# Performance work log

Measured on AMD Instinct MI355X. Metric: run time of the kernel, lower is better.

## Reference

```python
import jax, jax.numpy as jnp
import numpy as np

# Human3.6M 17-joint skeleton (parent of each joint; -1 = root)
_PARENTS = np.array([-1, 0, 1, 2, 0, 4, 5, 0, 7, 8, 9, 8, 11, 12, 8, 14, 15])
J = 17          # joints
C_OUT = 128     # out_features (per-channel adjacency count)
F_IN = 128      # in_features
B, T = 64, 243  # batch, frames
NEG = -9.0e15   # matches torch constant -9000000000000000.0


def _skeleton_indices():
    A = np.eye(J, dtype=np.float32)  # self-loops (SemGCN adjacency includes I)
    for i, p in enumerate(_PARENTS):
        if p >= 0:
            A[i, p] = 1.0
            A[p, i] = 1.0
    ii, jj = np.nonzero(A)  # row-major order, identical to torch adj>0 mask order
    return ii.astype(np.int32), jj.astype(np.int32)


def setup_inputs() -> dict:
    key = jax.random.key(0)
    kx, kw, ke = jax.random.split(key, 3)
    ii, jj = _skeleton_indices()  # nnz = 49
    x = jax.random.normal(kx, (B, T, J, F_IN), dtype=jnp.float32)
    # xavier_uniform with gain=1.414 over (2, in, out)
    bound = 1.414 * np.sqrt(6.0 / (F_IN + C_OUT))
    W = jax.random.uniform(kw, (2, F_IN, C_OUT), dtype=jnp.float32,
                           minval=-bound, maxval=bound)
    e = jax.random.uniform(ke, (C_OUT, ii.shape[0]), dtype=jnp.float32)
    return {"x": x, "W": W, "e": e,
            "idx_i": jnp.asarray(ii), "idx_j": jnp.asarray(jj)}


def reference(x, W, e, idx_i, idx_j):
    # x: [B,T,J,F_in], W: [2,F_in,C], e: [C,nnz]
    C = e.shape[0]
    nj = x.shape[2]
    h0 = jnp.einsum('btji,io->btjo', x, W[0])  # [B,T,J,C]
    h1 = jnp.einsum('btji,io->btjo', x, W[1])  # [B,T,J,C]
    # dense per-channel adjacency: masked scatter of e, then row softmax
    adj = jnp.full((C, nj, nj), NEG, dtype=x.dtype)
    adj = adj.at[:, idx_i, idx_j].set(e)
    adj = jax.nn.softmax(adj, axis=2)  # [C,J,J]
    # diagonal part: (adj*E) @ h0  ==  elementwise scale by diag entries
    d = jnp.diagonal(adj, axis1=1, axis2=2)        # [C,J]
    eye = jnp.eye(nj, dtype=x.dtype)
    off = adj * (1.0 - eye)                         # [C,J,J]
    out = h0 * d.T[None, None] + jnp.einsum('cjk,btkc->btjc', off, h1)
    return out  # [B,T,J,C]
```

## Files before the change

### kernel.cpp

```cpp
#include <hip/hip_runtime.h>

#define NJ   17
#define FD   128
#define NC   128
#define NNZ  49
#define FPT  16
#define XROW (NJ*FD)
#define WS_WT 65536

typedef __attribute__((ext_vector_type(8))) short bf16x8;
typedef __attribute__((ext_vector_type(4))) float f32x4;

__device__ __forceinline__ ushort f2bf(float f) {
  unsigned u = __float_as_uint(f);
  u = (u + 0x7fffu + ((u >> 16) & 1u)) >> 16;
  return (ushort)u;
}
__device__ __forceinline__ float bf2f(ushort s) {
  return __uint_as_float(((unsigned)s) << 16);
}
__device__ __forceinline__ unsigned cvtpk(float a, float b) {
  unsigned r;
  asm("v_cvt_pk_bf16_f32 %0, %1, %2" : "=v"(r) : "v"(a), "v"(b));
  return r;
}
__device__ __forceinline__ bf16x8 pack8(float4 a, float4 b) {
  union { unsigned u[4]; bf16x8 v; } r;
  r.u[0] = cvtpk(a.x, a.y); r.u[1] = cvtpk(a.z, a.w);
  r.u[2] = cvtpk(b.x, b.y); r.u[3] = cvtpk(b.z, b.w);
  return r.v;
}
__device__ __forceinline__ void axpy(f32x4& o, float s, f32x4 h) {
  o[0] += s * h[0]; o[1] += s * h[1]; o[2] += s * h[2]; o[3] += s * h[3];
}

struct CI { int col, dk, n, jl[3], kk[3]; };
constexpr CI TAB0[9] = {
  {0,  0, 3, {1,4,7}, {4,12,20}},
  {1,  5, 2, {0,2,0}, {1,7,0}},
  {2,  8, 2, {1,3,0}, {6,10,0}},
  {3, 11, 1, {2,0,0}, {9,0,0}},
  {4, 13, 2, {0,5,0}, {2,15,0}},
  {5, 16, 2, {4,6,0}, {14,18,0}},
  {6, 19, 1, {5,0,0}, {17,0,0}},
  {7, 21, 1, {0,0,0}, {3,0,0}},
  {8, -1, 1, {7,0,0}, {22,0,0}},
};
constexpr CI TAB1[10] = {
  {7, -1, 1, {0,0,0}, {23,0,0}},
  {8, 24, 3, {1,3,6}, {28,33,41}},
  {9, 29, 2, {0,2,0}, {25,31,0}},
  {10,32, 1, {1,0,0}, {30,0,0}},
  {11,34, 2, {0,4,0}, {26,36,0}},
  {12,37, 2, {3,5,0}, {35,39,0}},
  {13,40, 1, {4,0,0}, {38,0,0}},
  {14,42, 2, {0,7,0}, {27,44,0}},
  {15,45, 2, {6,8,0}, {43,47,0}},
  {16,48, 1, {7,0,0}, {46,0,0}},
};
constexpr int RP[NJ + 1] = {0,4,7,10,12,15,18,20,23,28,31,33,36,39,41,44,47,49};

__global__ void prep_pack_kernel(const float* __restrict__ W,
                                 const float* __restrict__ e,
                                 bf16x8* __restrict__ Wpack,
                                 ushort* __restrict__ wt) {
  const int tid = threadIdx.x;
  if (blockIdx.x < 16) {
    const int idx = blockIdx.x * 256 + tid, n = idx >> 4, kb = idx & 15;
    const float* Wp = W + (size_t)(n >> 7) * (FD * NC) + (n & 127);
    bf16x8 v;
#pragma unroll
    for (int q = 0; q < 8; ++q) v[q] = (short)f2bf(Wp[(size_t)(kb * 8 + q) * NC]);
    Wpack[idx] = v;
  } else if (tid < NC) {
    const int c = tid;
    for (int j = 0; j < NJ; ++j) {
      const int k0 = RP[j], k1 = RP[j + 1];
      float m = -1e30f;
      for (int k = k0; k < k1; ++k) m = fmaxf(m, e[c * NNZ + k]);
      float s = 0.f;
      for (int k = k0; k < k1; ++k) s += expf(e[c * NNZ + k] - m);
      const float inv = 1.f / s;
      for (int k = k0; k < k1; ++k) wt[c * 64 + k] = f2bf(expf(e[c * NNZ + k] - m) * inv);
    }
    for (int k = NNZ; k < 64; ++k) wt[c * 64 + k] = 0;
  }
}

template <int HALF>
__device__ __forceinline__ void half_work(const float* __restrict__ xt,
                                          float* __restrict__ ob,
                                          const bf16x8* __restrict__ Wpack,
                                          const ushort* __restrict__ wt,
                                          short* xs, int tid) {
  constexpr int COL0 = HALF ? 7 : 0;
  constexpr int NCOL = HALF ? 10 : 9;
  constexpr int JN   = HALF ? 9 : 8;
  constexpr int JB   = HALF ? 8 : 0;
  constexpr int NCI  = HALF ? 10 : 9;
  constexpr int NGRP = FPT * NCOL * 16;
  const CI* TT = HALF ? TAB1 : TAB0;

  const int w = tid >> 6, lane = tid & 63, l15 = lane & 15, l4 = lane >> 4;
  const int cb = w * 16;
  const int c  = cb + l15;

  float4 v[10];
#pragma unroll
  for (int i = 0; i < 5; ++i) {
    const int g = tid + i * 512;
    if (NGRP % 512 == 0 || g < NGRP) {
      const int fr = g / (NCOL * 16), rem = g - fr * (NCOL * 16);
      const float* sp = xt + (size_t)fr * XROW + COL0 * FD + rem * 8;
      v[2 * i]     = *(const float4*)(sp);
      v[2 * i + 1] = *(const float4*)(sp + 4);
    }
  }

  bf16x8 bfr[2][4];
#pragma unroll
  for (int sel = 0; sel < 2; ++sel)
#pragma unroll
    for (int ks = 0; ks < 4; ++ks)
      bfr[sel][ks] = Wpack[(sel * 128 + c) * 16 + ks * 4 + l4];
  bf16x8 wtp[7];
#pragma unroll
  for (int r = 0; r < 7; ++r)
    wtp[r] = *(const bf16x8*)(wt + c * 64 + r * 8);

#pragma unroll
  for (int i = 0; i < 5; ++i) {
    const int g = tid + i * 512;
    if (NGRP % 512 == 0 || g < NGRP) {
      const int fr = g / (NCOL * 16);
      const int byte = (g * 16) ^ ((fr & 7) << 4);
      *(bf16x8*)((char*)xs + byte) = pack8(v[2 * i], v[2 * i + 1]);
    }
  }
  __syncthreads();

  f32x4 oa[JN];
#pragma unroll
  for (int j = 0; j < JN; ++j) oa[j] = (f32x4){0.f, 0.f, 0.f, 0.f};

#pragma unroll
  for (int ci = 0; ci < NCI; ++ci) {
    const int lc = TT[ci].col - COL0, dk = TT[ci].dk, nn = TT[ci].n;
    bf16x8 af[4];
#pragma unroll
    for (int ks = 0; ks < 4; ++ks) {
      const int byte = l15 * (NCOL * 256) + lc * 256 +
                       (((ks * 4 + l4) * 16) ^ ((l15 & 7) << 4));
      af[ks] = *(const bf16x8*)((const char*)xs + byte);
    }
    f32x4 h1 = (f32x4){0.f, 0.f, 0.f, 0.f};
#pragma unroll
    for (int ks = 0; ks < 4; ++ks)
      h1 = __builtin_amdgcn_mfma_f32_16x16x32_bf16(af[ks], bfr[1][ks], h1, 0, 0, 0);
    if (dk >= 0) {
      f32x4 h0 = (f32x4){0.f, 0.f, 0.f, 0.f};
#pragma unroll
      for (int ks = 0; ks < 4; ++ks)
        h0 = __builtin_amdgcn_mfma_f32_16x16x32_bf16(af[ks], bfr[0][ks], h0, 0, 0, 0);
      axpy(oa[TT[ci].col - JB], bf2f((ushort)wtp[dk >> 3][dk & 7]), h0);
    }
#pragma unroll
    for (int o = 0; o < 3; ++o)
      if (o < nn)
        axpy(oa[TT[ci].jl[o]], bf2f((ushort)wtp[TT[ci].kk[o] >> 3][TT[ci].kk[o] & 7]), h1);
  }

#pragma unroll
  for (int j = 0; j < JN; ++j)
#pragma unroll
    for (int q = 0; q < 4; ++q)
      ob[(size_t)(l4 * 4 + q) * XROW + (JB + j) * FD + c] = oa[j][q];
}

__global__ __launch_bounds__(512, 4) void fused_kernel(
    const float*  __restrict__ x,
    const bf16x8* __restrict__ Wpack,
    const ushort* __restrict__ wt,
    float*        __restrict__ out) {
  __shared__ __align__(16) short xs[FPT * 10 * FD];
  const int tile = blockIdx.x >> 1;
  const float* xt = x + (size_t)tile * (FPT * XROW);
  float* ob = out + (size_t)tile * (FPT * XROW);
  if (blockIdx.x & 1) half_work<1>(xt, ob, Wpack, wt, xs, threadIdx.x);
  else                half_work<0>(xt, ob, Wpack, wt, xs, threadIdx.x);
}

extern "C" void kernel_launch(void* const* d_in, const int* in_sizes, int n_in,
                              void* d_out, int out_size, void* d_ws, size_t ws_size,
                              hipStream_t stream) {
  const float* x = (const float*)d_in[0];
  const float* W = (const float*)d_in[1];
  const float* e = (const float*)d_in[2];
  float* out = (float*)d_out;

  bf16x8* Wpack = (bf16x8*)d_ws;
  ushort* wt    = (ushort*)((char*)d_ws + WS_WT);

  prep_pack_kernel<<<17, 256, 0, stream>>>(W, e, Wpack, wt);

  const int frames = in_sizes[0] / XROW;
  const int ntiles = frames / FPT;
  fused_kernel<<<ntiles * 2, 512, 0, stream>>>(x, Wpack, wt, out);
}
```

Measured before the change: 99.81 us.

## Process two tiles per block with register prefetch of the next tile

Measured after the change: 163.0 us. 1.63x slower.

```diff
diff --git a/kernel.cpp b/kernel.cpp
--- a/kernel.cpp
+++ b/kernel.cpp
@@ -6,6 +6,7 @@
 #define NNZ  49
 #define FPT  16
 #define XROW (NJ*FD)
+#define TPB  2
 #define WS_WT 65536
 
 typedef __attribute__((ext_vector_type(8))) short bf16x8;
@@ -33,6 +34,12 @@
 __device__ __forceinline__ void axpy(f32x4& o, float s, f32x4 h) {
   o[0] += s * h[0]; o[1] += s * h[1]; o[2] += s * h[2]; o[3] += s * h[3];
 }
+
+#define BAR() do {                                          \
+    asm volatile("s_waitcnt lgkmcnt(0)" ::: "memory");      \
+    __builtin_amdgcn_s_barrier();                           \
+    __builtin_amdgcn_sched_barrier(0);                      \
+  } while (0)
 
 struct CI { int col, dk, n, jl[3], kk[3]; };
 constexpr CI TAB0[9] = {
@@ -88,34 +95,20 @@
 }
 
 template <int HALF>
-__device__ __forceinline__ void half_work(const float* __restrict__ xt,
-                                          float* __restrict__ ob,
-                                          const bf16x8* __restrict__ Wpack,
-                                          const ushort* __restrict__ wt,
-                                          short* xs, int tid) {
+__device__ __forceinline__ void body(const float* __restrict__ x,
+                                     const bf16x8* __restrict__ Wpack,
+                                     const ushort* __restrict__ wt,
+                                     float* __restrict__ out,
+                                     short* xs, int slot, int tid) {
   constexpr int COL0 = HALF ? 7 : 0;
   constexpr int NCOL = HALF ? 10 : 9;
   constexpr int JN   = HALF ? 9 : 8;
   constexpr int JB   = HALF ? 8 : 0;
-  constexpr int NCI  = HALF ? 10 : 9;
   constexpr int NGRP = FPT * NCOL * 16;
   const CI* TT = HALF ? TAB1 : TAB0;
 
   const int w = tid >> 6, lane = tid & 63, l15 = lane & 15, l4 = lane >> 4;
-  const int cb = w * 16;
-  const int c  = cb + l15;
-
-  float4 v[10];
-#pragma unroll
-  for (int i = 0; i < 5; ++i) {
-    const int g = tid + i * 512;
-    if (NGRP % 512 == 0 || g < NGRP) {
-      const int fr = g / (NCOL * 16), rem = g - fr * (NCOL * 16);
-      const float* sp = xt + (size_t)fr * XROW + COL0 * FD + rem * 8;
-      v[2 * i]     = *(const float4*)(sp);
-      v[2 * i + 1] = *(const float4*)(sp + 4);
-    }
-  }
+  const int c = w * 16 + l15;
 
   bf16x8 bfr[2][4];
 #pragma unroll
@@ -128,53 +121,85 @@
   for (int r = 0; r < 7; ++r)
     wtp[r] = *(const bf16x8*)(wt + c * 64 + r * 8);
 
-#pragma unroll
-  for (int i = 0; i < 5; ++i) {
-    const int g = tid + i * 512;
-    if (NGRP % 512 == 0 || g < NGRP) {
-      const int fr = g / (NCOL * 16);
-      const int byte = (g * 16) ^ ((fr & 7) << 4);
-      *(bf16x8*)((char*)xs + byte) = pack8(v[2 * i], v[2 * i + 1]);
+  float4 v[10];
+
+#define LOADX(T) do {                                                     \
+    const float* xp_ = x + (size_t)(T) * (FPT * XROW) + COL0 * FD;        \
+    _Pragma("unroll")                                                     \
+    for (int i_ = 0; i_ < 5; ++i_) {                                      \
+      int g_ = tid + i_ * 512;                                            \
+      if (g_ > NGRP - 1) g_ = NGRP - 1;                                   \
+      const int fr_ = g_ / (NCOL * 16), rem_ = g_ - fr_ * (NCOL * 16);    \
+      const float* sp_ = xp_ + (size_t)fr_ * XROW + rem_ * 8;             \
+      v[2 * i_]     = *(const float4*)(sp_);                              \
+      v[2 * i_ + 1] = *(const float4*)(sp_ + 4);                          \
+    }                                                                     \
+  } while (0)
+
+#define STAGE() do {                                                      \
+    _Pragma("unroll")                                                     \
+    for (int i_ = 0; i_ < 5; ++i_) {                                      \
+      const int g_ = tid + i_ * 512;                                      \
+      if (NGRP % 512 == 0 || g_ < NGRP) {                                 \
+        const int fr_ = g_ / (NCOL * 16);                                 \
+        const int byte_ = (g_ * 16) ^ ((fr_ & 7) << 4);                   \
+        *(bf16x8*)((char*)xs + byte_) = pack8(v[2 * i_], v[2 * i_ + 1]);  \
+      }                                                                   \
+    }                                                                     \
+  } while (0)
+
+  const int t0 = slot * TPB;
+  LOADX(t0);
+
+#pragma unroll
+  for (int i = 0; i < TPB; ++i) {
+    const int t = t0 + i;
+
+    BAR();
+    STAGE();
+    BAR();
+    if (i + 1 < TPB) LOADX(t + 1);
+
+    f32x4 oa[JN];
+#pragma unroll
+    for (int j = 0; j < JN; ++j) oa[j] = (f32x4){0.f, 0.f, 0.f, 0.f};
+
+#pragma unroll
+    for (int ci = 0; ci < NCOL; ++ci) {
+      const int lc = TT[ci].col - COL0, dk = TT[ci].dk, nn = TT[ci].n;
+      bf16x8 af[4];
+#pragma unroll
+      for (int ks = 0; ks < 4; ++ks) {
+        const int byte = l15 * (NCOL * 256) + lc * 256 +
+                         (((ks * 4 + l4) * 16) ^ ((l15 & 7) << 4));
+        af[ks] = *(const bf16x8*)((const char*)xs + byte);
+      }
+      f32x4 h1 = (f32x4){0.f, 0.f, 0.f, 0.f};
+#pragma unroll
+      for (int ks = 0; ks < 4; ++ks)
+        h1 = __builtin_amdgcn_mfma_f32_16x16x32_bf16(af[ks], bfr[1][ks], h1, 0, 0, 0);
+      if (dk >= 0) {
+        f32x4 h0 = (f32x4){0.f, 0.f, 0.f, 0.f};
+#pragma unroll
+        for (int ks = 0; ks < 4; ++ks)
+          h0 = __builtin_amdgcn_mfma_f32_16x16x32_bf16(af[ks], bfr[0][ks], h0, 0, 0, 0);
+        axpy(oa[TT[ci].col - JB], bf2f((ushort)wtp[dk >> 3][dk & 7]), h0);
+      }
+#pragma unroll
+      for (int o = 0; o < 3; ++o)
+        if (o < nn)
+          axpy(oa[TT[ci].jl[o]], bf2f((ushort)wtp[TT[ci].kk[o] >> 3][TT[ci].kk[o] & 7]), h1);
     }
+
+    float* ob = out + (size_t)t * (FPT * XROW);
+#pragma unroll
+    for (int j = 0; j < JN; ++j)
+#pragma unroll
+      for (int q = 0; q < 4; ++q)
+        ob[(size_t)(l4 * 4 + q) * XROW + (JB + j) * FD + c] = oa[j][q];
   }
-  __syncthreads();
-
-  f32x4 oa[JN];
-#pragma unroll
-  for (int j = 0; j < JN; ++j) oa[j] = (f32x4){0.f, 0.f, 0.f, 0.f};
-
-#pragma unroll
-  for (int ci = 0; ci < NCI; ++ci) {
-    const int lc = TT[ci].col - COL0, dk = TT[ci].dk, nn = TT[ci].n;
-    bf16x8 af[4];
-#pragma unroll
-    for (int ks = 0; ks < 4; ++ks) {
-      const int byte = l15 * (NCOL * 256) + lc * 256 +
-                       (((ks * 4 + l4) * 16) ^ ((l15 & 7) << 4));
-      af[ks] = *(const bf16x8*)((const char*)xs + byte);
-    }
-    f32x4 h1 = (f32x4){0.f, 0.f, 0.f, 0.f};
-#pragma unroll
-    for (int ks = 0; ks < 4; ++ks)
-      h1 = __builtin_amdgcn_mfma_f32_16x16x32_bf16(af[ks], bfr[1][ks], h1, 0, 0, 0);
-    if (dk >= 0) {
-      f32x4 h0 = (f32x4){0.f, 0.f, 0.f, 0.f};
-#pragma unroll
-      for (int ks = 0; ks < 4; ++ks)
-        h0 = __builtin_amdgcn_mfma_f32_16x16x32_bf16(af[ks], bfr[0][ks], h0, 0, 0, 0);
-      axpy(oa[TT[ci].col - JB], bf2f((ushort)wtp[dk >> 3][dk & 7]), h0);
-    }
-#pragma unroll
-    for (int o = 0; o < 3; ++o)
-      if (o < nn)
-        axpy(oa[TT[ci].jl[o]], bf2f((ushort)wtp[TT[ci].kk[o] >> 3][TT[ci].kk[o] & 7]), h1);
-  }
-
-#pragma unroll
-  for (int j = 0; j < JN; ++j)
-#pragma unroll
-    for (int q = 0; q < 4; ++q)
-      ob[(size_t)(l4 * 4 + q) * XROW + (JB + j) * FD + c] = oa[j][q];
+#undef LOADX
+#undef STAGE
 }
 
 __global__ __launch_bounds__(512, 4) void fused_kernel(
@@ -183,11 +208,9 @@
     const ushort* __restrict__ wt,
     float*        __restrict__ out) {
   __shared__ __align__(16) short xs[FPT * 10 * FD];
-  const int tile = blockIdx.x >> 1;
-  const float* xt = x + (size_t)tile * (FPT * XROW);
-  float* ob = out + (size_t)tile * (FPT * XROW);
-  if (blockIdx.x & 1) half_work<1>(xt, ob, Wpack, wt, xs, threadIdx.x);
-  else                half_work<0>(xt, ob, Wpack, wt, xs, threadIdx.x);
+  const int slot = blockIdx.x >> 1;
+  if (blockIdx.x & 1) body<1>(x, Wpack, wt, out, xs, slot, threadIdx.x);
+  else                body<0>(x, Wpack, wt, out, xs, slot, threadIdx.x);
 }
 
 extern "C" void kernel_launch(void* const* d_in, const int* in_sizes, int n_in,
@@ -205,5 +228,6 @@
 
   const int frames = in_sizes[0] / XROW;
   const int ntiles = frames / FPT;
-  fused_kernel<<<ntiles * 2, 512, 0, stream>>>(x, Wpack, wt, out);
-}
+  const int blocks = (ntiles / TPB) * 2;
+  fused_kernel<<<blocks, 512, 0, stream>>>(x, Wpack, wt, out);
+}
```

## Double-buffer x tiles via global_load_lds across K-quarters and two tiles per block

Applied to the files above, without the earlier changes.

After: 223.1 us. 123% more time.

```diff
diff --git a/kernel.cpp b/kernel.cpp
--- a/kernel.cpp
+++ b/kernel.cpp
@@ -6,6 +6,8 @@
 #define NNZ  49
 #define FPT  16
 #define XROW (NJ*FD)
+#define TPB  2
+#define BUFB 20736
 #define WS_WT 65536
 
 typedef __attribute__((ext_vector_type(8))) short bf16x8;
@@ -24,15 +26,21 @@
   asm("v_cvt_pk_bf16_f32 %0, %1, %2" : "=v"(r) : "v"(a), "v"(b));
   return r;
 }
-__device__ __forceinline__ bf16x8 pack8(float4 a, float4 b) {
+__device__ __forceinline__ bf16x8 pack8(f32x4 a, f32x4 b) {
   union { unsigned u[4]; bf16x8 v; } r;
-  r.u[0] = cvtpk(a.x, a.y); r.u[1] = cvtpk(a.z, a.w);
-  r.u[2] = cvtpk(b.x, b.y); r.u[3] = cvtpk(b.z, b.w);
+  r.u[0] = cvtpk(a[0], a[1]); r.u[1] = cvtpk(a[2], a[3]);
+  r.u[2] = cvtpk(b[0], b[1]); r.u[3] = cvtpk(b[2], b[3]);
   return r.v;
 }
 __device__ __forceinline__ void axpy(f32x4& o, float s, f32x4 h) {
   o[0] += s * h[0]; o[1] += s * h[1]; o[2] += s * h[2]; o[3] += s * h[3];
 }
+
+#define WVM(N) do { asm volatile("s_waitcnt vmcnt(" #N ")" ::: "memory"); \
+                    __builtin_amdgcn_sched_barrier(0); } while (0)
+#define BARR() do { asm volatile("s_waitcnt lgkmcnt(0)" ::: "memory"); \
+                    __builtin_amdgcn_s_barrier(); \
+                    __builtin_amdgcn_sched_barrier(0); } while (0)
 
 struct CI { int col, dk, n, jl[3], kk[3]; };
 constexpr CI TAB0[9] = {
@@ -87,81 +95,27 @@
   }
 }
 
-template <int HALF>
-__device__ __forceinline__ void half_work(const float* __restrict__ xt,
-                                          float* __restrict__ ob,
-                                          const bf16x8* __restrict__ Wpack,
-                                          const ushort* __restrict__ wt,
-                                          short* xs, int tid) {
+template <int HALF, int P, int JN>
+__device__ __forceinline__ void cphase(const char* bb, int foff, int l4,
+                                       const bf16x8 (&bfr)[2][4],
+                                       const bf16x8 (&wtp)[7],
+                                       f32x4 (&oa)[JN]) {
+  constexpr int KQ   = P & 3;
   constexpr int COL0 = HALF ? 7 : 0;
   constexpr int NCOL = HALF ? 10 : 9;
-  constexpr int JN   = HALF ? 9 : 8;
   constexpr int JB   = HALF ? 8 : 0;
-  constexpr int NCI  = HALF ? 10 : 9;
-  constexpr int NGRP = FPT * NCOL * 16;
   const CI* TT = HALF ? TAB1 : TAB0;
-
-  const int w = tid >> 6, lane = tid & 63, l15 = lane & 15, l4 = lane >> 4;
-  const int cb = w * 16;
-  const int c  = cb + l15;
-
-  float4 v[10];
-#pragma unroll
-  for (int i = 0; i < 5; ++i) {
-    const int g = tid + i * 512;
-    if (NGRP % 512 == 0 || g < NGRP) {
-      const int fr = g / (NCOL * 16), rem = g - fr * (NCOL * 16);
-      const float* sp = xt + (size_t)fr * XROW + COL0 * FD + rem * 8;
-      v[2 * i]     = *(const float4*)(sp);
-      v[2 * i + 1] = *(const float4*)(sp + 4);
-    }
-  }
-
-  bf16x8 bfr[2][4];
-#pragma unroll
-  for (int sel = 0; sel < 2; ++sel)
-#pragma unroll
-    for (int ks = 0; ks < 4; ++ks)
-      bfr[sel][ks] = Wpack[(sel * 128 + c) * 16 + ks * 4 + l4];
-  bf16x8 wtp[7];
-#pragma unroll
-  for (int r = 0; r < 7; ++r)
-    wtp[r] = *(const bf16x8*)(wt + c * 64 + r * 8);
-
-#pragma unroll
-  for (int i = 0; i < 5; ++i) {
-    const int g = tid + i * 512;
-    if (NGRP % 512 == 0 || g < NGRP) {
-      const int fr = g / (NCOL * 16);
-      const int byte = (g * 16) ^ ((fr & 7) << 4);
-      *(bf16x8*)((char*)xs + byte) = pack8(v[2 * i], v[2 * i + 1]);
-    }
-  }
-  __syncthreads();
-
-  f32x4 oa[JN];
-#pragma unroll
-  for (int j = 0; j < JN; ++j) oa[j] = (f32x4){0.f, 0.f, 0.f, 0.f};
-
-#pragma unroll
-  for (int ci = 0; ci < NCI; ++ci) {
+  const char* fb = bb + foff;
+#pragma unroll
+  for (int ci = 0; ci < NCOL; ++ci) {
     const int lc = TT[ci].col - COL0, dk = TT[ci].dk, nn = TT[ci].n;
-    bf16x8 af[4];
-#pragma unroll
-    for (int ks = 0; ks < 4; ++ks) {
-      const int byte = l15 * (NCOL * 256) + lc * 256 +
-                       (((ks * 4 + l4) * 16) ^ ((l15 & 7) << 4));
-      af[ks] = *(const bf16x8*)((const char*)xs + byte);
-    }
-    f32x4 h1 = (f32x4){0.f, 0.f, 0.f, 0.f};
-#pragma unroll
-    for (int ks = 0; ks < 4; ++ks)
-      h1 = __builtin_amdgcn_mfma_f32_16x16x32_bf16(af[ks], bfr[1][ks], h1, 0, 0, 0);
+    const f32x4 lo = *(const f32x4*)(fb + lc * 128 + l4 * 32);
+    const f32x4 hi = *(const f32x4*)(fb + lc * 128 + l4 * 32 + 16);
+    const bf16x8 af = pack8(lo, hi);
+    const f32x4 z = (f32x4){0.f, 0.f, 0.f, 0.f};
+    const f32x4 h1 = __builtin_amdgcn_mfma_f32_16x16x32_bf16(af, bfr[1][KQ], z, 0, 0, 0);
     if (dk >= 0) {
-      f32x4 h0 = (f32x4){0.f, 0.f, 0.f, 0.f};
-#pragma unroll
-      for (int ks = 0; ks < 4; ++ks)
-        h0 = __builtin_amdgcn_mfma_f32_16x16x32_bf16(af[ks], bfr[0][ks], h0, 0, 0, 0);
+      const f32x4 h0 = __builtin_amdgcn_mfma_f32_16x16x32_bf16(af, bfr[0][KQ], z, 0, 0, 0);
       axpy(oa[TT[ci].col - JB], bf2f((ushort)wtp[dk >> 3][dk & 7]), h0);
     }
 #pragma unroll
@@ -169,12 +123,101 @@
       if (o < nn)
         axpy(oa[TT[ci].jl[o]], bf2f((ushort)wtp[TT[ci].kk[o] >> 3][TT[ci].kk[o] & 7]), h1);
   }
-
-#pragma unroll
-  for (int j = 0; j < JN; ++j)
-#pragma unroll
-    for (int q = 0; q < 4; ++q)
-      ob[(size_t)(l4 * 4 + q) * XROW + (JB + j) * FD + c] = oa[j][q];
+}
+
+template <int HALF>
+__device__ __forceinline__ void run(const float* __restrict__ x,
+                                    const bf16x8* __restrict__ Wpack,
+                                    const ushort* __restrict__ wt,
+                                    float* __restrict__ out,
+                                    char* xs, int slot, int tid) {
+  constexpr int COL0 = HALF ? 7 : 0;
+  constexpr int JN   = HALF ? 9 : 8;
+  constexpr int JB   = HALF ? 8 : 0;
+  const int w = tid >> 6, lane = tid & 63, l15 = lane & 15, l4 = lane >> 4;
+  const int c = w * 16 + l15;
+
+  bf16x8 bfr[2][4];
+#pragma unroll
+  for (int sel = 0; sel < 2; ++sel)
+#pragma unroll
+    for (int ks = 0; ks < 4; ++ks)
+      bfr[sel][ks] = Wpack[(sel * 128 + c) * 16 + ks * 4 + l4];
+  bf16x8 wtp[7];
+#pragma unroll
+  for (int r = 0; r < 7; ++r)
+    wtp[r] = *(const bf16x8*)(wt + c * 64 + r * 8);
+
+  f32x4 oa[JN];
+#pragma unroll
+  for (int j = 0; j < JN; ++j) oa[j] = (f32x4){0.f, 0.f, 0.f, 0.f};
+
+  const int foff = HALF ? l15 * 1296 : (l15 >> 1) * 2320 + (l15 & 1) * 1152;
+
+  auto issue = [&](int p) {
+    const int t = p >> 2, kq = p & 3;
+    char* dst = xs + (p & 1) * BUFB;
+    const float* gf0 = x + ((size_t)(slot * TPB + t) * FPT + 2 * w) * XROW +
+                       COL0 * FD + kq * 32;
+    const float* gf1 = gf0 + XROW;
+    if (HALF) {
+      char* d0 = dst + (2 * w) * 1296;
+      __builtin_amdgcn_global_load_lds(gf0 + (lane >> 3) * FD + (lane & 7) * 4,
+                                       (void*)d0, 16, 0, 0);
+      __builtin_amdgcn_global_load_lds(gf0 + (8 + (lane >> 5)) * FD + (lane & 31),
+                                       (void*)(d0 + 1024), 4, 0, 0);
+      __builtin_amdgcn_global_load_lds(gf1 + (lane >> 3) * FD + (lane & 7) * 4,
+                                       (void*)(d0 + 1296), 16, 0, 0);
+      __builtin_amdgcn_global_load_lds(gf1 + (8 + (lane >> 5)) * FD + (lane & 31),
+                                       (void*)(d0 + 1296 + 1024), 4, 0, 0);
+    } else {
+      char* pb = dst + w * 2320;
+      const float* s2 = (lane < 8)
+          ? gf0 + 8 * FD + lane * 4
+          : gf1 + ((lane * 16 - 128) >> 7) * FD + (((lane * 16 - 128) & 127) >> 2);
+      __builtin_amdgcn_global_load_lds(gf0 + (lane >> 3) * FD + (lane & 7) * 4,
+                                       (void*)pb, 16, 0, 0);
+      __builtin_amdgcn_global_load_lds(s2, (void*)(pb + 1024), 16, 0, 0);
+      __builtin_amdgcn_global_load_lds(gf1 + (7 + (lane >> 5)) * FD + (lane & 31),
+                                       (void*)(pb + 2048), 4, 0, 0);
+    }
+  };
+
+  auto stores = [&](int t) {
+    float* ob = out + (size_t)(slot * TPB + t) * FPT * XROW;
+#pragma unroll
+    for (int j = 0; j < JN; ++j) {
+#pragma unroll
+      for (int q = 0; q < 4; ++q)
+        ob[(size_t)(l4 * 4 + q) * XROW + (JB + j) * FD + c] = oa[j][q];
+      oa[j] = (f32x4){0.f, 0.f, 0.f, 0.f};
+    }
+  };
+
+  issue(0); issue(1);
+  if (HALF) WVM(4); else WVM(3);
+  BARR();
+
+  char* b0 = xs;
+  char* b1 = xs + BUFB;
+
+  cphase<HALF, 0, JN>(b0, foff, l4, bfr, wtp, oa);
+  BARR(); issue(2); if (HALF) WVM(4); else WVM(3); BARR();
+  cphase<HALF, 1, JN>(b1, foff, l4, bfr, wtp, oa);
+  BARR(); issue(3); if (HALF) WVM(4); else WVM(3); BARR();
+  cphase<HALF, 2, JN>(b0, foff, l4, bfr, wtp, oa);
+  BARR(); issue(4); if (HALF) WVM(4); else WVM(3); BARR();
+  cphase<HALF, 3, JN>(b1, foff, l4, bfr, wtp, oa);
+  stores(0);
+  BARR(); issue(5); if (HALF) WVM(40); else WVM(35); BARR();
+  cphase<HALF, 4, JN>(b0, foff, l4, bfr, wtp, oa);
+  BARR(); issue(6); if (HALF) WVM(4); else WVM(3); BARR();
+  cphase<HALF, 5, JN>(b1, foff, l4, bfr, wtp, oa);
+  BARR(); issue(7); if (HALF) WVM(4); else WVM(3); BARR();
+  cphase<HALF, 6, JN>(b0, foff, l4, bfr, wtp, oa);
+  BARR(); WVM(0); BARR();
+  cphase<HALF, 7, JN>(b1, foff, l4, bfr, wtp, oa);
+  stores(1);
 }
 
 __global__ __launch_bounds__(512, 4) void fused_kernel(
@@ -182,12 +225,10 @@
     const bf16x8* __restrict__ Wpack,
     const ushort* __restrict__ wt,
     float*        __restrict__ out) {
-  __shared__ __align__(16) short xs[FPT * 10 * FD];
-  const int tile = blockIdx.x >> 1;
-  const float* xt = x + (size_t)tile * (FPT * XROW);
-  float* ob = out + (size_t)tile * (FPT * XROW);
-  if (blockIdx.x & 1) half_work<1>(xt, ob, Wpack, wt, xs, threadIdx.x);
-  else                half_work<0>(xt, ob, Wpack, wt, xs, threadIdx.x);
+  __shared__ __align__(16) char xs[2 * BUFB];
+  const int slot = blockIdx.x >> 1;
+  if (blockIdx.x & 1) run<1>(x, Wpack, wt, out, xs, slot, threadIdx.x);
+  else                run<0>(x, Wpack, wt, out, xs, slot, threadIdx.x);
 }
 
 extern "C" void kernel_launch(void* const* d_in, const int* in_sizes, int n_in,
@@ -204,6 +245,6 @@
   prep_pack_kernel<<<17, 256, 0, stream>>>(W, e, Wpack, wt);
 
   const int frames = in_sizes[0] / XROW;
-  const int ntiles = frames / FPT;
-  fused_kernel<<<ntiles * 2, 512, 0, stream>>>(x, Wpack, wt, out);
-}
+  const int slots  = frames / (FPT * TPB);
+  fused_kernel<<<slots * 2, 512, 0, stream>>>(x, Wpack, wt, out);
+}
```

## Split blocks by channel group, pipeline x staging, store finished joints early

Applied to the files above, without the earlier changes.

Result: slower. 107.4 us (+7.6%).

```diff
diff --git a/kernel.cpp b/kernel.cpp
--- a/kernel.cpp
+++ b/kernel.cpp
@@ -60,6 +60,11 @@
 };
 constexpr int RP[NJ + 1] = {0,4,7,10,12,15,18,20,23,28,31,33,36,39,41,44,47,49};
 
+constexpr int FL0[9][2]  = {{-1,-1},{-1,-1},{1,-1},{2,3},{-1,-1},
+                            {4,-1},{5,6},{0,-1},{7,-1}};
+constexpr int FL1[10][2] = {{-1,-1},{-1,-1},{-1,-1},{1,2},{-1,-1},
+                            {3,-1},{4,5},{0,-1},{6,-1},{7,8}};
+
 __global__ void prep_pack_kernel(const float* __restrict__ W,
                                  const float* __restrict__ e,
                                  bf16x8* __restrict__ Wpack,
@@ -88,34 +93,22 @@
 }
 
 template <int HALF>
-__device__ __forceinline__ void half_work(const float* __restrict__ xt,
-                                          float* __restrict__ ob,
-                                          const bf16x8* __restrict__ Wpack,
-                                          const ushort* __restrict__ wt,
-                                          short* xs, int tid) {
+__device__ __forceinline__ void run(const float* __restrict__ x,
+                                    const bf16x8* __restrict__ Wpack,
+                                    const ushort* __restrict__ wt,
+                                    float* __restrict__ out,
+                                    short* xs, int tile, int cg, int tid) {
   constexpr int COL0 = HALF ? 7 : 0;
   constexpr int NCOL = HALF ? 10 : 9;
   constexpr int JN   = HALF ? 9 : 8;
   constexpr int JB   = HALF ? 8 : 0;
-  constexpr int NCI  = HALF ? 10 : 9;
-  constexpr int NGRP = FPT * NCOL * 16;
+  constexpr int NW   = HALF ? 5 : 3;
+  constexpr int WB   = HALF ? 2 : 0;
   const CI* TT = HALF ? TAB1 : TAB0;
+  const int (*FL)[2] = HALF ? FL1 : FL0;
 
   const int w = tid >> 6, lane = tid & 63, l15 = lane & 15, l4 = lane >> 4;
-  const int cb = w * 16;
-  const int c  = cb + l15;
-
-  float4 v[10];
-#pragma unroll
-  for (int i = 0; i < 5; ++i) {
-    const int g = tid + i * 512;
-    if (NGRP % 512 == 0 || g < NGRP) {
-      const int fr = g / (NCOL * 16), rem = g - fr * (NCOL * 16);
-      const float* sp = xt + (size_t)fr * XROW + COL0 * FD + rem * 8;
-      v[2 * i]     = *(const float4*)(sp);
-      v[2 * i + 1] = *(const float4*)(sp + 4);
-    }
-  }
+  const int c = cg * 64 + w * 16 + l15;
 
   bf16x8 bfr[2][4];
 #pragma unroll
@@ -123,33 +116,50 @@
 #pragma unroll
     for (int ks = 0; ks < 4; ++ks)
       bfr[sel][ks] = Wpack[(sel * 128 + c) * 16 + ks * 4 + l4];
-  bf16x8 wtp[7];
-#pragma unroll
-  for (int r = 0; r < 7; ++r)
-    wtp[r] = *(const bf16x8*)(wt + c * 64 + r * 8);
-
-#pragma unroll
-  for (int i = 0; i < 5; ++i) {
-    const int g = tid + i * 512;
-    if (NGRP % 512 == 0 || g < NGRP) {
-      const int fr = g / (NCOL * 16);
-      const int byte = (g * 16) ^ ((fr & 7) << 4);
-      *(bf16x8*)((char*)xs + byte) = pack8(v[2 * i], v[2 * i + 1]);
-    }
-  }
+  bf16x8 wtp[NW];
+#pragma unroll
+  for (int r = 0; r < NW; ++r)
+    wtp[r] = *(const bf16x8*)(wt + c * 64 + (WB + r) * 8);
+
+  const float* xt = x + (size_t)tile * (FPT * XROW) + COL0 * FD;
+  float4 v[12];
+
+#define LOADP(I, S) do {                                                  \
+    const int g_ = tid + (I) * 256;                                       \
+    const int fr_ = g_ / (NCOL * 16), rem_ = g_ - fr_ * (NCOL * 16);      \
+    const float* sp_ = xt + (size_t)fr_ * XROW + rem_ * 8;                \
+    v[(S)] = *(const float4*)sp_; v[(S) + 1] = *(const float4*)(sp_ + 4); \
+  } while (0)
+#define STWP(I, S) do {                                                   \
+    const int g_ = tid + (I) * 256;                                       \
+    const int fr_ = g_ / (NCOL * 16);                                     \
+    const int byte_ = (g_ * 16) ^ ((fr_ & 7) << 4);                       \
+    *(bf16x8*)((char*)xs + byte_) = pack8(v[(S)], v[(S) + 1]);            \
+  } while (0)
+
+  LOADP(0, 0); LOADP(1, 2); LOADP(2, 4);
+  LOADP(3, 6); LOADP(4, 8); LOADP(5, 10);
+  STWP(0, 0); STWP(1, 2); STWP(2, 4);
+  LOADP(6, 0); LOADP(7, 2); LOADP(8, 4);
+  STWP(3, 6); STWP(4, 8); STWP(5, 10);
+  if (HALF) LOADP(9, 6);
+  STWP(6, 0); STWP(7, 2); STWP(8, 4);
+  if (HALF) STWP(9, 6);
   __syncthreads();
 
   f32x4 oa[JN];
 #pragma unroll
   for (int j = 0; j < JN; ++j) oa[j] = (f32x4){0.f, 0.f, 0.f, 0.f};
 
-#pragma unroll
-  for (int ci = 0; ci < NCI; ++ci) {
-    const int lc = TT[ci].col - COL0, dk = TT[ci].dk, nn = TT[ci].n;
+  float* const ob = out + (size_t)tile * (FPT * XROW);
+
+#pragma unroll
+  for (int ci = 0; ci < NCOL; ++ci) {
+    const int dk = TT[ci].dk, nn = TT[ci].n;
     bf16x8 af[4];
 #pragma unroll
     for (int ks = 0; ks < 4; ++ks) {
-      const int byte = l15 * (NCOL * 256) + lc * 256 +
+      const int byte = l15 * (NCOL * 256) + ci * 256 +
                        (((ks * 4 + l4) * 16) ^ ((l15 & 7) << 4));
       af[ks] = *(const bf16x8*)((const char*)xs + byte);
     }
@@ -162,32 +172,39 @@
 #pragma unroll
       for (int ks = 0; ks < 4; ++ks)
         h0 = __builtin_amdgcn_mfma_f32_16x16x32_bf16(af[ks], bfr[0][ks], h0, 0, 0, 0);
-      axpy(oa[TT[ci].col - JB], bf2f((ushort)wtp[dk >> 3][dk & 7]), h0);
+      axpy(oa[TT[ci].col - JB], bf2f((ushort)wtp[(dk >> 3) - WB][dk & 7]), h0);
     }
 #pragma unroll
     for (int o = 0; o < 3; ++o)
       if (o < nn)
-        axpy(oa[TT[ci].jl[o]], bf2f((ushort)wtp[TT[ci].kk[o] >> 3][TT[ci].kk[o] & 7]), h1);
+        axpy(oa[TT[ci].jl[o]],
+             bf2f((ushort)wtp[(TT[ci].kk[o] >> 3) - WB][TT[ci].kk[o] & 7]), h1);
+
+#pragma unroll
+    for (int fi = 0; fi < 2; ++fi) {
+      const int fj = FL[ci][fi];
+      if (fj >= 0) {
+#pragma unroll
+        for (int q = 0; q < 4; ++q)
+          ob[(size_t)(l4 * 4 + q) * XROW + (JB + fj) * FD + c] = oa[fj][q];
+      }
+    }
   }
-
-#pragma unroll
-  for (int j = 0; j < JN; ++j)
-#pragma unroll
-    for (int q = 0; q < 4; ++q)
-      ob[(size_t)(l4 * 4 + q) * XROW + (JB + j) * FD + c] = oa[j][q];
-}
-
-__global__ __launch_bounds__(512, 4) void fused_kernel(
+#undef LOADP
+#undef STWP
+}
+
+__global__ __launch_bounds__(256, 4) void fused_kernel(
     const float*  __restrict__ x,
     const bf16x8* __restrict__ Wpack,
     const ushort* __restrict__ wt,
     float*        __restrict__ out) {
   __shared__ __align__(16) short xs[FPT * 10 * FD];
-  const int tile = blockIdx.x >> 1;
-  const float* xt = x + (size_t)tile * (FPT * XROW);
-  float* ob = out + (size_t)tile * (FPT * XROW);
-  if (blockIdx.x & 1) half_work<1>(xt, ob, Wpack, wt, xs, threadIdx.x);
-  else                half_work<0>(xt, ob, Wpack, wt, xs, threadIdx.x);
+  const int tile = blockIdx.x >> 2;
+  const int half = (blockIdx.x >> 1) & 1;
+  const int cg   = blockIdx.x & 1;
+  if (half) run<1>(x, Wpack, wt, out, xs, tile, cg, threadIdx.x);
+  else      run<0>(x, Wpack, wt, out, xs, tile, cg, threadIdx.x);
 }
 
 extern "C" void kernel_launch(void* const* d_in, const int* in_sizes, int n_in,
@@ -205,5 +222,5 @@
 
   const int frames = in_sizes[0] / XROW;
   const int ntiles = frames / FPT;
-  fused_kernel<<<ntiles * 2, 512, 0, stream>>>(x, Wpack, wt, out);
-}
+  fused_kernel<<<ntiles * 4, 256, 0, stream>>>(x, Wpack, wt, out);
+}
```
